# Kernel optimization log

Hardware: AMD Instinct MI355X
Metric: run time of the kernel (lower is better)

## Reference

```python
import jax, jax.numpy as jnp
import numpy as np


def _depthwise3x3(x_nhwc, w):
    # w: (3, 3, 1, C) — depthwise conv, padding=1, matches torch Conv2d(groups=C)
    return jax.lax.conv_general_dilated(
        x_nhwc, w, window_strides=(1, 1), padding='SAME',
        dimension_numbers=('NHWC', 'HWIO', 'NHWC'),
        feature_group_count=x_nhwc.shape[-1])


def _stripe_attn(q, k, v, lepe_w, B, H, W, nh, hd, ss, axis, scale):
    # q/k/v: (B, H, W, nh*hd); axis 0 = horizontal stripes, 1 = vertical
    pad_h = (-H) % ss if axis == 0 else 0
    pad_w = (-W) % ss if axis == 1 else 0
    if pad_h or pad_w:
        pad = ((0, 0), (0, pad_h), (0, pad_w), (0, 0))
        q, k, v = jnp.pad(q, pad), jnp.pad(k, pad), jnp.pad(v, pad)
    Hp, Wp = q.shape[1], q.shape[2]
    lepe = _depthwise3x3(v, lepe_w)  # (B, Hp, Wp, nh*hd)

    if axis == 0:
        nS = Hp // ss
        def to_win(t):  # -> (B*nS*Wp, nh, ss, hd)
            t = t.reshape(B, nS, ss, Wp, nh, hd)
            return t.transpose(0, 1, 3, 4, 2, 5).reshape(B * nS * Wp, nh, ss, hd)
    else:
        nS = Wp // ss
        def to_win(t):  # -> (B*Hp*nS, nh, ss, hd)
            t = t.reshape(B, Hp, nS, ss, nh, hd)
            return t.transpose(0, 1, 2, 4, 3, 5).reshape(B * Hp * nS, nh, ss, hd)

    qw, kw, vw, lw = to_win(q), to_win(k), to_win(v), to_win(lepe)
    attn = jax.nn.softmax(jnp.einsum('wnqd,wnkd->wnqk', qw, kw) / scale, axis=-1)
    out = jnp.einsum('wnqk,wnkd->wnqd', attn, vw) + lw  # (Wnum, nh, ss, hd)

    if axis == 0:
        out = out.transpose(0, 2, 1, 3).reshape(B, nS, Wp, ss, nh * hd)
        out = out.transpose(0, 1, 3, 2, 4).reshape(B, Hp, Wp, nh * hd)
    else:
        out = out.transpose(0, 2, 1, 3).reshape(B, Hp, nS, ss, nh * hd)
        out = out.reshape(B, Hp, Wp, nh * hd)
    return out[:, :H, :W, :].reshape(B, H * W, nh * hd)


def setup_inputs() -> dict:
    key = jax.random.key(0)
    ks = jax.random.split(key, 6)
    B, H, W, dim, n_heads, ss = 8, 64, 64, 512, 16, 8
    half = dim // 2
    x = jax.random.normal(ks[0], (B, H * W, dim), dtype=jnp.float32)
    w_qkv = jax.random.normal(ks[1], (3 * dim, dim), dtype=jnp.float32) * 0.02
    w_proj = jax.random.normal(ks[2], (dim, dim), dtype=jnp.float32) * 0.02
    b_proj = jnp.zeros((dim,), dtype=jnp.float32)
    lepe_h_w = jax.random.normal(ks[3], (3, 3, 1, half), dtype=jnp.float32) * 0.1
    lepe_v_w = jax.random.normal(ks[4], (3, 3, 1, half), dtype=jnp.float32) * 0.1
    return {"x": x, "w_qkv": w_qkv, "w_proj": w_proj, "b_proj": b_proj,
            "lepe_h_w": lepe_h_w, "lepe_v_w": lepe_v_w, "H": H, "W": W}


def reference(x, w_qkv, w_proj, b_proj, lepe_h_w, lepe_v_w, H, W):
    B, L, C = x.shape
    n_heads, ss = 16, 8
    hd = C // n_heads
    scale = float(np.sqrt(hd))
    qkv = x @ w_qkv.T  # (B, L, 3C)
    q, k, v = jnp.split(qkv, 3, axis=-1)
    q = q.reshape(B, H, W, C)
    k = k.reshape(B, H, W, C)
    v = v.reshape(B, H, W, C)
    half = C // 2
    nh_h = n_heads // 2
    nh_v = n_heads - nh_h
    out_h = _stripe_attn(q[..., :half], k[..., :half], v[..., :half],
                         lepe_h_w, B, H, W, nh_h, hd, ss, axis=0, scale=scale)
    out_v = _stripe_attn(q[..., half:], k[..., half:], v[..., half:],
                         lepe_v_w, B, H, W, nh_v, hd, ss, axis=1, scale=scale)
    out = jnp.concatenate([out_h, out_v], axis=-1)
    return out @ w_proj.T + b_proj
```

## Files before the change

kernel.cpp:

```cpp
#include <hip/hip_runtime.h>
#include <hip/hip_bf16.h>
#include <stdint.h>

typedef _Float16 half2v __attribute__((ext_vector_type(2)));
typedef _Float16 half8v __attribute__((ext_vector_type(8)));
typedef uint32_t u32x4  __attribute__((ext_vector_type(4)));
typedef float    f32x4  __attribute__((ext_vector_type(4)));

__device__ __forceinline__ unsigned short f2h(float f) {
  _Float16 h = (_Float16)f;
  return __builtin_bit_cast(unsigned short, h);
}
__device__ __forceinline__ half2v bch2(uint32_t u) {
  return __builtin_bit_cast(half2v, u);
}
__device__ __forceinline__ uint32_t pkrtz_u32(float a, float b) {
  return __builtin_bit_cast(uint32_t, __builtin_amdgcn_cvt_pkrtz(a, b));
}

__device__ __forceinline__ int qkv_idx(int half, int b, int n, int h, int w) {
  int idx = half * 8388608 + (b * 8 + n) * 131072;
  idx += (half == 0) ? ((h >> 3) * 16384 + w * 256 + (h & 7) * 32)
                     : (h * 2048 + w * 32);
  return idx;
}

#define GLOAD_LDS16(gsrc, lbase)                                          \
  __builtin_amdgcn_global_load_lds(                                       \
      (const __attribute__((address_space(1))) uint32_t*)(gsrc),          \
      (__attribute__((address_space(3))) uint32_t*)(lbase), 16, 0, 0)

__global__ __launch_bounds__(256) void cvt_all(
    const float* __restrict__ x,
    const float* __restrict__ wqkv, const float* __restrict__ wproj,
    const float* __restrict__ lh,   const float* __restrict__ lv,
    unsigned short* __restrict__ ox,
    unsigned short* __restrict__ owqkv, unsigned short* __restrict__ owproj,
    unsigned short* __restrict__ owlep)
{
  int i = blockIdx.x * 256 + threadIdx.x;
  const float* src; unsigned short* dst; int off;
  if (i < 4194304)      { src = x;     dst = ox;           off = i; }
  else if ((i -= 4194304) < 196608) { src = wqkv;  dst = owqkv;  off = i; }
  else if ((i -= 196608) < 65536)   { src = wproj; dst = owproj; off = i; }
  else if ((i -= 65536) < 576)      { src = lh;    dst = owlep;  off = i; }
  else if ((i -= 576) < 576)        { src = lv;    dst = owlep + 2304; off = i; }
  else return;
  float4 f = reinterpret_cast<const float4*>(src)[off];
  ushort4 u;
  u.x = f2h(f.x); u.y = f2h(f.y); u.z = f2h(f.z); u.w = f2h(f.w);
  reinterpret_cast<ushort4*>(dst)[off] = u;
}

template<int MODE>
__global__ __launch_bounds__(512, 2) void gemm8(
    const unsigned short* __restrict__ A,
    const unsigned short* __restrict__ Bm,
    unsigned short* __restrict__ Cq,
    float* __restrict__ Cf,
    const float* __restrict__ bias,
    int M, int N)
{
  constexpr int K = 512;
  constexpr int NIT = 4;
  __shared__ unsigned short As[2][256 * 64];
  __shared__ unsigned short Bs[2][256 * 64];
  const int tid  = threadIdx.x;
  const int gn   = N >> 8;
  const int cpx  = gridDim.x >> 3;
  const int bid  = blockIdx.x;
  const int wgid = (bid & 7) * cpx + (bid >> 3);
  const int m0   = (wgid / gn) * 256;
  const int n0   = (wgid % gn) * 256;
  const int wave = tid >> 6, lane = tid & 63;
  const int wr  = wave >> 2;
  const int wcn = wave & 3;

  const int srow = tid >> 3;
  const int schk = ((tid & 7) ^ (srow & 7)) * 8;
  const size_t aSrc = (size_t)(m0 + srow) * K + schk;
  const size_t bSrc = (size_t)(n0 + srow) * K + schk;
  char* ldsA = (char*)(&As[0][0]) + (tid & ~63) * 16;
  char* ldsB = (char*)(&Bs[0][0]) + (tid & ~63) * 16;

#define SA_U(b, kt, u)                                                      \
  GLOAD_LDS16(A + aSrc + (size_t)(u) * 64 * K + (size_t)(kt) * 64,          \
              ldsA + (b) * 32768 + (u) * 8192)
#define SB_U(b, kt, u)                                                      \
  GLOAD_LDS16(Bm + bSrc + (size_t)(u) * 64 * K + (size_t)(kt) * 64,         \
              ldsB + (b) * 32768 + (u) * 8192)
#define BARS                                                                \
  __builtin_amdgcn_s_barrier();                                             \
  __builtin_amdgcn_sched_barrier(0)

  SA_U(0, 0, 0); SA_U(0, 0, 1); SA_U(0, 0, 2); SA_U(0, 0, 3);
  SB_U(0, 0, 0); SB_U(0, 0, 1); SB_U(0, 0, 2); SB_U(0, 0, 3);
  SB_U(1, 1, 0); SB_U(1, 1, 1); SB_U(1, 1, 2); SB_U(1, 1, 3);

  f32x4 acc[8][4];
  const f32x4 zero = {0.f, 0.f, 0.f, 0.f};
  #pragma unroll
  for (int i = 0; i < 8; ++i)
    #pragma unroll
    for (int j = 0; j < 4; ++j) acc[i][j] = zero;

  const int lr  = lane & 15;
  const int kg  = lane >> 4;
  const int ck0 = kg ^ (lr & 7);

  asm volatile("s_waitcnt vmcnt(4)" ::: "memory");
  BARS;

#define LD_AF(buf, mg, ks)                                                  \
  do {                                                                      \
    const unsigned short* ap = &As[buf][0] +                                \
        (wr * 128 + (mg) * 64 + lr) * 64 + (((ks) ? (ck0 ^ 4) : ck0)) * 8;  \
    af[0] = *(const half8v*)(ap);                                           \
    af[1] = *(const half8v*)(ap + 1024);                                    \
    af[2] = *(const half8v*)(ap + 2048);                                    \
    af[3] = *(const half8v*)(ap + 3072);                                    \
  } while (0)
#define LD_BF(buf, ks)                                                      \
  do {                                                                      \
    const unsigned short* bp = &Bs[buf][0] +                                \
        (wcn * 64 + lr) * 64 + (((ks) ? (ck0 ^ 4) : ck0)) * 8;              \
    bf[0] = *(const half8v*)(bp);                                           \
    bf[1] = *(const half8v*)(bp + 1024);                                    \
    bf[2] = *(const half8v*)(bp + 2048);                                    \
    bf[3] = *(const half8v*)(bp + 3072);                                    \
  } while (0)
#define MROW(mg, i)                                                         \
  acc[(mg)*4+(i)][0] = __builtin_amdgcn_mfma_f32_16x16x32_f16(bf[0], af[i], acc[(mg)*4+(i)][0], 0, 0, 0); \
  acc[(mg)*4+(i)][1] = __builtin_amdgcn_mfma_f32_16x16x32_f16(bf[1], af[i], acc[(mg)*4+(i)][1], 0, 0, 0); \
  acc[(mg)*4+(i)][2] = __builtin_amdgcn_mfma_f32_16x16x32_f16(bf[2], af[i], acc[(mg)*4+(i)][2], 0, 0, 0); \
  acc[(mg)*4+(i)][3] = __builtin_amdgcn_mfma_f32_16x16x32_f16(bf[3], af[i], acc[(mg)*4+(i)][3], 0, 0, 0);
#define MFMA16(mg)                                                          \
  do {                                                                      \
    __builtin_amdgcn_s_setprio(1);                                          \
    MROW(mg, 0); MROW(mg, 1); MROW(mg, 2); MROW(mg, 3);                     \
    __builtin_amdgcn_s_setprio(0);                                          \
  } while (0)

  for (int it2 = 0; it2 < NIT; ++it2) {
    const bool more = (it2 + 1 < NIT);
    const int keven = 2 * it2;
    half8v af[4], bf[4];
    LD_BF(0, 0); LD_AF(0, 0, 0);
    SA_U(1, keven + 1, 0); SA_U(1, keven + 1, 1);
    BARS;
    MFMA16(0);
    BARS;
    LD_AF(0, 1, 0);
    SA_U(1, keven + 1, 2); SA_U(1, keven + 1, 3);
    BARS;
    MFMA16(1);
    BARS;
    LD_BF(0, 1); LD_AF(0, 0, 1);
    BARS;
    MFMA16(0);
    BARS;
    LD_AF(0, 1, 1);
    if (more) {
      SB_U(0, keven + 2, 0); SB_U(0, keven + 2, 1);
      asm volatile("s_waitcnt vmcnt(2)" ::: "memory");
    } else {
      asm volatile("s_waitcnt vmcnt(0)" ::: "memory");
    }
    BARS;
    MFMA16(1);
    BARS;
    LD_BF(1, 0); LD_AF(1, 0, 0);
    if (more) { SB_U(0, keven + 2, 2); SB_U(0, keven + 2, 3); }
    BARS;
    MFMA16(0);
    BARS;
    LD_AF(1, 1, 0);
    if (more) { SA_U(0, keven + 2, 0); SA_U(0, keven + 2, 1); }
    BARS;
    MFMA16(1);
    BARS;
    LD_BF(1, 1); LD_AF(1, 0, 1);
    if (more) { SA_U(0, keven + 2, 2); SA_U(0, keven + 2, 3); }
    BARS;
    MFMA16(0);
    BARS;
    LD_AF(1, 1, 1);
    if (more) {
      SB_U(1, keven + 3, 0); SB_U(1, keven + 3, 1);
      SB_U(1, keven + 3, 2); SB_U(1, keven + 3, 3);
      asm volatile("s_waitcnt vmcnt(4)" ::: "memory");
    }
    BARS;
    MFMA16(1);
    BARS;
  }
#undef SA_U
#undef SB_U
#undef LD_AF
#undef LD_BF
#undef MROW
#undef MFMA16
#undef BARS

  const int cr = (lane >> 4) * 4;
  const int cc = lane & 15;

  if constexpr (MODE == 0) {
    #pragma unroll
    for (int j = 0; j < 4; ++j) {
      const int n = n0 + wcn * 64 + j * 16 + cr;
      const float4 b4 = *reinterpret_cast<const float4*>(bias + n);
      #pragma unroll
      for (int i = 0; i < 8; ++i) {
        const int m = m0 + wr * 128 + i * 16 + cc;
        float4 r;
        r.x = acc[i][j][0] + b4.x;
        r.y = acc[i][j][1] + b4.y;
        r.z = acc[i][j][2] + b4.z;
        r.w = acc[i][j][3] + b4.w;
        *reinterpret_cast<float4*>(Cf + (size_t)m * N + n) = r;
      }
    }
  } else {
    const int mb   = m0 + wr * 128;
    const int btok = mb >> 12;
    const int hr0  = (mb >> 6) & 63;
    #pragma unroll
    for (int j = 0; j < 4; ++j) {
      const int nb    = n0 + wcn * 64 + j * 16 + cr;
      const int tq    = nb >> 9;
      const int halfc = (nb >> 8) & 1;
      const int nn    = (nb & 255) >> 5;
      const int ch4   = nb & 31;
      const int headbase = tq * 16777216 + halfc * 8388608 +
                           (btok * 8 + nn) * 131072 + ch4;
      #pragma unroll
      for (int i = 0; i < 8; ++i) {
        const int hrow = hr0 + (i >> 2);
        const int wpix = (i & 3) * 16 + cc;
        const int off = halfc ? (hrow * 2048 + wpix * 32)
                              : ((hrow >> 3) * 16384 + wpix * 256 + (hrow & 7) * 32);
        uint2 r;
        r.x = pkrtz_u32(acc[i][j][0], acc[i][j][1]);
        r.y = pkrtz_u32(acc[i][j][2], acc[i][j][3]);
        *reinterpret_cast<uint2*>(Cq + headbase + off) = r;
      }
    }
  }
}

__global__ __launch_bounds__(256) void gemm_proj(
    const unsigned short* __restrict__ A,
    const unsigned short* __restrict__ B,
    float* __restrict__ Cf,
    const float* __restrict__ bias)
{
  constexpr int K = 512, N = 512;
  __shared__ unsigned short As[2][128 * 32];
  __shared__ unsigned short Bs[2][128 * 32];
  const int tid  = threadIdx.x;
  const int gn   = N >> 7;
  const int cpx  = gridDim.x >> 3;
  const int bid  = blockIdx.x;
  const int wgid = (bid & 7) * cpx + (bid >> 3);
  const int m0   = (wgid / gn) * 128;
  const int n0   = (wgid % gn) * 128;
  const int wave = tid >> 6, lane = tid & 63;
  const int wr = wave >> 1, wc = wave & 1;
  const int sr = tid >> 2;
  const int sc = ((tid & 3) ^ ((tid >> 3) & 3)) * 8;
  const size_t aBase0 = (size_t)(m0 + sr) * K + sc;
  const size_t aBase1 = (size_t)(m0 + 64 + sr) * K + sc;
  const size_t bBase0 = (size_t)(n0 + sr) * K + sc;
  const size_t bBase1 = (size_t)(n0 + 64 + sr) * K + sc;
  char* ldsA = (char*)(&As[0][0]) + (tid & ~63) * 16;
  char* ldsB = (char*)(&Bs[0][0]) + (tid & ~63) * 16;

#define STAGE_P(bsel, kofs)                                        \
  do {                                                             \
    GLOAD_LDS16(A + aBase0 + (kofs), ldsA + (bsel) * 8192);        \
    GLOAD_LDS16(A + aBase1 + (kofs), ldsA + (bsel) * 8192 + 4096); \
    GLOAD_LDS16(B + bBase0 + (kofs), ldsB + (bsel) * 8192);        \
    GLOAD_LDS16(B + bBase1 + (kofs), ldsB + (bsel) * 8192 + 4096); \
  } while (0)

  STAGE_P(0, 0);

  f32x4 acc[4][4];
  const f32x4 zero = {0.f, 0.f, 0.f, 0.f};
  #pragma unroll
  for (int i = 0; i < 4; ++i)
    #pragma unroll
    for (int j = 0; j < 4; ++j) acc[i][j] = zero;

  const int lr   = lane & 15;
  const int slot = (lane >> 4) ^ ((lr >> 1) & 3);

  auto compute = [&](const unsigned short* Asb, const unsigned short* Bsb) {
    half8v af[4], bfr[4];
    #pragma unroll
    for (int i = 0; i < 4; ++i)
      af[i] = *reinterpret_cast<const half8v*>(Asb + (wr * 64 + i * 16 + lr) * 32 + slot * 8);
    #pragma unroll
    for (int j = 0; j < 4; ++j)
      bfr[j] = *reinterpret_cast<const half8v*>(Bsb + (wc * 64 + j * 16 + lr) * 32 + slot * 8);
    __builtin_amdgcn_s_setprio(1);
    #pragma unroll
    for (int i = 0; i < 4; ++i)
      #pragma unroll
      for (int j = 0; j < 4; ++j)
        acc[i][j] = __builtin_amdgcn_mfma_f32_16x16x32_f16(bfr[j], af[i], acc[i][j], 0, 0, 0);
    __builtin_amdgcn_s_setprio(0);
  };

  const int nt = K >> 5;
  for (int t = 0; t < nt - 1; ++t) {
    STAGE_P((t + 1) & 1, (t + 1) * 32);
    asm volatile("s_waitcnt vmcnt(4)" ::: "memory");
    __builtin_amdgcn_s_barrier();
    __builtin_amdgcn_sched_barrier(0);
    compute(&As[t & 1][0], &Bs[t & 1][0]);
    __builtin_amdgcn_s_barrier();
    __builtin_amdgcn_sched_barrier(0);
  }
  asm volatile("s_waitcnt vmcnt(0)" ::: "memory");
  __builtin_amdgcn_s_barrier();
  __builtin_amdgcn_sched_barrier(0);
  compute(&As[(nt - 1) & 1][0], &Bs[(nt - 1) & 1][0]);
#undef STAGE_P

  const int cr = (lane >> 4) * 4;
  const int cc = lane & 15;
  #pragma unroll
  for (int j = 0; j < 4; ++j) {
    const int n = n0 + wc * 64 + j * 16 + cr;
    const float4 b4 = *reinterpret_cast<const float4*>(bias + n);
    #pragma unroll
    for (int i = 0; i < 4; ++i) {
      const int m = m0 + wr * 64 + i * 16 + cc;
      float4 r;
      r.x = acc[i][j][0] + b4.x;
      r.y = acc[i][j][1] + b4.y;
      r.z = acc[i][j][2] + b4.z;
      r.w = acc[i][j][3] + b4.w;
      *reinterpret_cast<float4*>(Cf + (size_t)m * N + n) = r;
    }
  }
}

__global__ __launch_bounds__(256) void attn_lepe(
    const unsigned short* __restrict__ qkvp,
    const unsigned short* __restrict__ wlep,
    unsigned short* __restrict__ outp)
{
  const int gw   = (int)((blockIdx.x * 256 + threadIdx.x) >> 6);
  const int lane = threadIdx.x & 63;
  const int half = gw >> 14;
  const int id   = gw & 16383;
  const int b    = id >> 11;
  const int n    = (id >> 8) & 7;
  int h0, w0;
  if (half == 0) { h0 = ((id >> 5) & 7) * 8; w0 = (id & 31) * 2; }
  else           { h0 = ((id >> 3) & 31) * 2; w0 = (id & 7) * 8; }
  const int baseA = qkv_idx(half, b, n, h0, w0);
  const int dWin  = (half == 0) ? 256 : 2048;
  const int baseB = baseA + dWin;

  const int qr = lane >> 3, kr = lane & 7;
  const unsigned short* qA = qkvp + baseA + qr * 32;
  const unsigned short* kA = qkvp + 16777216 + baseA + kr * 32;
  float sA = 0.f, sB = 0.f;
  #pragma unroll
  for (int c = 0; c < 4; ++c) {
    const u32x4 qa = *reinterpret_cast<const u32x4*>(qA + c * 8);
    const u32x4 ka = *reinterpret_cast<const u32x4*>(kA + c * 8);
    const u32x4 qb = *reinterpret_cast<const u32x4*>(qA + dWin + c * 8);
    const u32x4 kb = *reinterpret_cast<const u32x4*>(kA + dWin + c * 8);
    #pragma unroll
    for (int e = 0; e < 4; ++e) {
      sA = __builtin_amdgcn_fdot2(bch2(qa[e]), bch2(ka[e]), sA, false);
      sB = __builtin_amdgcn_fdot2(bch2(qb[e]), bch2(kb[e]), sB, false);
    }
  }
  const float scl = 0.17677669529663687f;
  const float pA = __expf(sA * scl);
  const float pB = __expf(sB * scl);
  float denA = pA, denB = pB;
  denA += __shfl_xor(denA, 1); denA += __shfl_xor(denA, 2); denA += __shfl_xor(denA, 4);
  denB += __shfl_xor(denB, 1); denB += __shfl_xor(denB, 2); denB += __shfl_xor(denB, 4);
  const float aAv = pA * __builtin_amdgcn_rcpf(denA);
  const float aBv = pB * __builtin_amdgcn_rcpf(denB);
  const uint32_t adu = pkrtz_u32(aAv, aBv);

  const int dgrp = lane & 3;
  const int win  = (lane >> 2) & 1;
  const int qr2  = lane >> 3;
  const int d0   = dgrp * 8;
  const int mybase = win ? baseB : baseA;
  const unsigned short* vwin = qkvp + 33554432 + mybase;

  half2v o01 = {0,0}, o23 = {0,0}, o45 = {0,0}, o67 = {0,0};
  #pragma unroll
  for (int k = 0; k < 8; ++k) {
    const uint32_t pairw = (uint32_t)__shfl((int)adu, qr2 * 8 + k);
    const half2v ph = bch2(pairw);
    const _Float16 av = win ? ph.y : ph.x;
    const half2v ak2 = {av, av};
    const u32x4 vv = *reinterpret_cast<const u32x4*>(vwin + k * 32 + d0);
    o01 += ak2 * bch2(vv[0]);
    o23 += ak2 * bch2(vv[1]);
    o45 += ak2 * bch2(vv[2]);
    o67 += ak2 * bch2(vv[3]);
  }

  const int hq = (half == 0) ? (h0 + qr2) : (h0 + win);
  const int wq = (half == 0) ? (w0 + win) : (w0 + qr2);
  const unsigned short* vplane = qkvp + 33554432;
  const unsigned short* wl = wlep + half * 2304 + n * 32 + d0;
  half2v l01 = {0,0}, l23 = {0,0}, l45 = {0,0}, l67 = {0,0};
  #pragma unroll
  for (int dy = -1; dy <= 1; ++dy) {
    #pragma unroll
    for (int dx = -1; dx <= 1; ++dx) {
      const int hh = hq + dy, ww = wq + dx;
      u32x4 vv = {0u, 0u, 0u, 0u};
      if ((unsigned)hh < 64u && (unsigned)ww < 64u)
        vv = *reinterpret_cast<const u32x4*>(vplane + qkv_idx(half, b, n, hh, ww) + d0);
      const u32x4 wt = *reinterpret_cast<const u32x4*>(wl + ((dy + 1) * 3 + dx + 1) * 256);
      l01 += bch2(wt[0]) * bch2(vv[0]);
      l23 += bch2(wt[1]) * bch2(vv[1]);
      l45 += bch2(wt[2]) * bch2(vv[2]);
      l67 += bch2(wt[3]) * bch2(vv[3]);
    }
  }

  const int m = b * 4096 + hq * 64 + wq;
  const int chan0 = half * 256 + n * 32;
  u32x4 r;
  r[0] = __builtin_bit_cast(uint32_t, (half2v)(o01 + l01));
  r[1] = __builtin_bit_cast(uint32_t, (half2v)(o23 + l23));
  r[2] = __builtin_bit_cast(uint32_t, (half2v)(o45 + l45));
  r[3] = __builtin_bit_cast(uint32_t, (half2v)(o67 + l67));
  *reinterpret_cast<u32x4*>(outp + (size_t)m * 512 + chan0 + d0) = r;
}

extern "C" void kernel_launch(void* const* d_in, const int* in_sizes, int n_in,
                              void* d_out, int out_size, void* d_ws, size_t ws_size,
                              hipStream_t stream) {
  const float* x      = (const float*)d_in[0];
  const float* w_qkv  = (const float*)d_in[1];
  const float* w_proj = (const float*)d_in[2];
  const float* b_proj = (const float*)d_in[3];
  const float* lepe_h = (const float*)d_in[4];
  const float* lepe_v = (const float*)d_in[5];
  float* out = (float*)d_out;

  char* ws = (char*)d_ws;
  unsigned short* qkv_p   = (unsigned short*)ws;
  unsigned short* xh      = (unsigned short*)(ws + 100663296);
  unsigned short* wqkv_h  = (unsigned short*)(ws + 134217728);
  unsigned short* wproj_h = (unsigned short*)(ws + 135790592);
  unsigned short* wlep_h  = (unsigned short*)(ws + 136314880);

  cvt_all<<<17413, 256, 0, stream>>>(x, w_qkv, w_proj, lepe_h, lepe_v,
                                     xh, wqkv_h, wproj_h, wlep_h);

  gemm8<1><<<768, 512, 0, stream>>>(
      xh, wqkv_h, qkv_p, nullptr, nullptr, 32768, 1536);

  attn_lepe<<<8192, 256, 0, stream>>>(qkv_p, wlep_h, xh);

  gemm_proj<<<1024, 256, 0, stream>>>(xh, wproj_h, out, b_proj);
}
```

Measured before the change: 172.5 us.

## Make QKV GEMM persistent over three N tiles with prefetch during epilogue

The QKV GEMM now launches 256 workgroups instead of 768. Each workgroup processes three consecutive 256-wide N tiles for one M tile, so block launch and prologue costs are paid once per workgroup. The next tile's A and B loads are issued before the current tile's epilogue stores, which overlaps the store phase with global-to-LDS prefetch. The cost is lower parallelism: 256 blocks on a 256-CU part gives a single wave of work with no tail balancing, and A is re-read three times per block, though likely from cache.

Result: no change. 169.8 us, median of 2 (-1.6%).

```diff
diff --git a/kernel.cpp b/kernel.cpp
--- a/kernel.cpp
+++ b/kernel.cpp
@@ -52,26 +52,22 @@
   reinterpret_cast<ushort4*>(dst)[off] = u;
 }
 
-template<int MODE>
-__global__ __launch_bounds__(512, 2) void gemm8(
+__global__ __launch_bounds__(512, 2) void gemm8p(
     const unsigned short* __restrict__ A,
     const unsigned short* __restrict__ Bm,
-    unsigned short* __restrict__ Cq,
-    float* __restrict__ Cf,
-    const float* __restrict__ bias,
-    int M, int N)
+    unsigned short* __restrict__ Cq)
 {
   constexpr int K = 512;
   constexpr int NIT = 4;
   __shared__ unsigned short As[2][256 * 64];
   __shared__ unsigned short Bs[2][256 * 64];
   const int tid  = threadIdx.x;
-  const int gn   = N >> 8;
   const int cpx  = gridDim.x >> 3;
   const int bid  = blockIdx.x;
   const int wgid = (bid & 7) * cpx + (bid >> 3);
-  const int m0   = (wgid / gn) * 256;
-  const int n0   = (wgid % gn) * 256;
+  const int mt   = wgid >> 1;
+  const int nh   = wgid & 1;
+  const int m0   = mt * 256;
   const int wave = tid >> 6, lane = tid & 63;
   const int wr  = wave >> 2;
   const int wcn = wave & 3;
@@ -79,37 +75,29 @@
   const int srow = tid >> 3;
   const int schk = ((tid & 7) ^ (srow & 7)) * 8;
   const size_t aSrc = (size_t)(m0 + srow) * K + schk;
-  const size_t bSrc = (size_t)(n0 + srow) * K + schk;
+  size_t bSrc = (size_t)(nh * 768 + srow) * K + schk;
   char* ldsA = (char*)(&As[0][0]) + (tid & ~63) * 16;
   char* ldsB = (char*)(&Bs[0][0]) + (tid & ~63) * 16;
 
 #define SA_U(b, kt, u)                                                      \
   GLOAD_LDS16(A + aSrc + (size_t)(u) * 64 * K + (size_t)(kt) * 64,          \
               ldsA + (b) * 32768 + (u) * 8192)
-#define SB_U(b, kt, u)                                                      \
-  GLOAD_LDS16(Bm + bSrc + (size_t)(u) * 64 * K + (size_t)(kt) * 64,         \
+#define SB_U(b, kt, u, bS)                                                  \
+  GLOAD_LDS16(Bm + (bS) + (size_t)(u) * 64 * K + (size_t)(kt) * 64,         \
               ldsB + (b) * 32768 + (u) * 8192)
 #define BARS                                                                \
   __builtin_amdgcn_s_barrier();                                             \
   __builtin_amdgcn_sched_barrier(0)
 
   SA_U(0, 0, 0); SA_U(0, 0, 1); SA_U(0, 0, 2); SA_U(0, 0, 3);
-  SB_U(0, 0, 0); SB_U(0, 0, 1); SB_U(0, 0, 2); SB_U(0, 0, 3);
-  SB_U(1, 1, 0); SB_U(1, 1, 1); SB_U(1, 1, 2); SB_U(1, 1, 3);
-
-  f32x4 acc[8][4];
-  const f32x4 zero = {0.f, 0.f, 0.f, 0.f};
-  #pragma unroll
-  for (int i = 0; i < 8; ++i)
-    #pragma unroll
-    for (int j = 0; j < 4; ++j) acc[i][j] = zero;
+  SB_U(0, 0, 0, bSrc); SB_U(0, 0, 1, bSrc); SB_U(0, 0, 2, bSrc); SB_U(0, 0, 3, bSrc);
+  SB_U(1, 1, 0, bSrc); SB_U(1, 1, 1, bSrc); SB_U(1, 1, 2, bSrc); SB_U(1, 1, 3, bSrc);
+  asm volatile("s_waitcnt vmcnt(4)" ::: "memory");
+  BARS;
 
   const int lr  = lane & 15;
   const int kg  = lane >> 4;
   const int ck0 = kg ^ (lr & 7);
-
-  asm volatile("s_waitcnt vmcnt(4)" ::: "memory");
-  BARS;
 
 #define LD_AF(buf, mg, ks)                                                  \
   do {                                                                      \
@@ -141,58 +129,112 @@
     __builtin_amdgcn_s_setprio(0);                                          \
   } while (0)
 
-  for (int it2 = 0; it2 < NIT; ++it2) {
-    const bool more = (it2 + 1 < NIT);
-    const int keven = 2 * it2;
-    half8v af[4], bf[4];
-    LD_BF(0, 0); LD_AF(0, 0, 0);
-    SA_U(1, keven + 1, 0); SA_U(1, keven + 1, 1);
-    BARS;
-    MFMA16(0);
-    BARS;
-    LD_AF(0, 1, 0);
-    SA_U(1, keven + 1, 2); SA_U(1, keven + 1, 3);
-    BARS;
-    MFMA16(1);
-    BARS;
-    LD_BF(0, 1); LD_AF(0, 0, 1);
-    BARS;
-    MFMA16(0);
-    BARS;
-    LD_AF(0, 1, 1);
-    if (more) {
-      SB_U(0, keven + 2, 0); SB_U(0, keven + 2, 1);
-      asm volatile("s_waitcnt vmcnt(2)" ::: "memory");
-    } else {
+  f32x4 acc[8][4];
+  const f32x4 zero = {0.f, 0.f, 0.f, 0.f};
+
+  #pragma unroll 1
+  for (int pass = 0; pass < 3; ++pass) {
+    const int n0 = (nh * 3 + pass) * 256;
+    #pragma unroll
+    for (int i = 0; i < 8; ++i)
+      #pragma unroll
+      for (int j = 0; j < 4; ++j) acc[i][j] = zero;
+
+    for (int it2 = 0; it2 < NIT; ++it2) {
+      const bool more = (it2 + 1 < NIT);
+      const int keven = 2 * it2;
+      half8v af[4], bf[4];
+      LD_BF(0, 0); LD_AF(0, 0, 0);
+      SA_U(1, keven + 1, 0); SA_U(1, keven + 1, 1);
+      BARS;
+      MFMA16(0);
+      BARS;
+      LD_AF(0, 1, 0);
+      SA_U(1, keven + 1, 2); SA_U(1, keven + 1, 3);
+      BARS;
+      MFMA16(1);
+      BARS;
+      LD_BF(0, 1); LD_AF(0, 0, 1);
+      BARS;
+      MFMA16(0);
+      BARS;
+      LD_AF(0, 1, 1);
+      if (more) {
+        SB_U(0, keven + 2, 0, bSrc); SB_U(0, keven + 2, 1, bSrc);
+        asm volatile("s_waitcnt vmcnt(2)" ::: "memory");
+      } else {
+        asm volatile("s_waitcnt vmcnt(0)" ::: "memory");
+      }
+      BARS;
+      MFMA16(1);
+      BARS;
+      LD_BF(1, 0); LD_AF(1, 0, 0);
+      if (more) { SB_U(0, keven + 2, 2, bSrc); SB_U(0, keven + 2, 3, bSrc); }
+      BARS;
+      MFMA16(0);
+      BARS;
+      LD_AF(1, 1, 0);
+      if (more) { SA_U(0, keven + 2, 0); SA_U(0, keven + 2, 1); }
+      BARS;
+      MFMA16(1);
+      BARS;
+      LD_BF(1, 1); LD_AF(1, 0, 1);
+      if (more) { SA_U(0, keven + 2, 2); SA_U(0, keven + 2, 3); }
+      BARS;
+      MFMA16(0);
+      BARS;
+      LD_AF(1, 1, 1);
+      if (more) {
+        SB_U(1, keven + 3, 0, bSrc); SB_U(1, keven + 3, 1, bSrc);
+        SB_U(1, keven + 3, 2, bSrc); SB_U(1, keven + 3, 3, bSrc);
+        asm volatile("s_waitcnt vmcnt(4)" ::: "memory");
+      }
+      BARS;
+      MFMA16(1);
+      BARS;
+    }
+
+    if (pass < 2) {
+      const size_t bSrcN = bSrc + (size_t)256 * K;
+      SA_U(0, 0, 0); SA_U(0, 0, 1); SA_U(0, 0, 2); SA_U(0, 0, 3);
+      SB_U(0, 0, 0, bSrcN); SB_U(0, 0, 1, bSrcN); SB_U(0, 0, 2, bSrcN); SB_U(0, 0, 3, bSrcN);
+      SB_U(1, 1, 0, bSrcN); SB_U(1, 1, 1, bSrcN); SB_U(1, 1, 2, bSrcN); SB_U(1, 1, 3, bSrcN);
+      bSrc = bSrcN;
+    }
+
+    {
+      const int cr = (lane >> 4) * 4;
+      const int cc = lane & 15;
+      const int mb   = m0 + wr * 128;
+      const int btok = mb >> 12;
+      const int hr0  = (mb >> 6) & 63;
+      #pragma unroll
+      for (int j = 0; j < 4; ++j) {
+        const int nb    = n0 + wcn * 64 + j * 16 + cr;
+        const int tq    = nb >> 9;
+        const int halfc = (nb >> 8) & 1;
+        const int nn    = (nb & 255) >> 5;
+        const int ch4   = nb & 31;
+        const int headbase = tq * 16777216 + halfc * 8388608 +
+                             (btok * 8 + nn) * 131072 + ch4;
+        #pragma unroll
+        for (int i = 0; i < 8; ++i) {
+          const int hrow = hr0 + (i >> 2);
+          const int wpix = (i & 3) * 16 + cc;
+          const int off = halfc ? (hrow * 2048 + wpix * 32)
+                                : ((hrow >> 3) * 16384 + wpix * 256 + (hrow & 7) * 32);
+          uint2 r;
+          r.x = pkrtz_u32(acc[i][j][0], acc[i][j][1]);
+          r.y = pkrtz_u32(acc[i][j][2], acc[i][j][3]);
+          *reinterpret_cast<uint2*>(Cq + headbase + off) = r;
+        }
+      }
+    }
+
+    if (pass < 2) {
       asm volatile("s_waitcnt vmcnt(0)" ::: "memory");
-    }
-    BARS;
-    MFMA16(1);
-    BARS;
-    LD_BF(1, 0); LD_AF(1, 0, 0);
-    if (more) { SB_U(0, keven + 2, 2); SB_U(0, keven + 2, 3); }
-    BARS;
-    MFMA16(0);
-    BARS;
-    LD_AF(1, 1, 0);
-    if (more) { SA_U(0, keven + 2, 0); SA_U(0, keven + 2, 1); }
-    BARS;
-    MFMA16(1);
-    BARS;
-    LD_BF(1, 1); LD_AF(1, 0, 1);
-    if (more) { SA_U(0, keven + 2, 2); SA_U(0, keven + 2, 3); }
-    BARS;
-    MFMA16(0);
-    BARS;
-    LD_AF(1, 1, 1);
-    if (more) {
-      SB_U(1, keven + 3, 0); SB_U(1, keven + 3, 1);
-      SB_U(1, keven + 3, 2); SB_U(1, keven + 3, 3);
-      asm volatile("s_waitcnt vmcnt(4)" ::: "memory");
-    }
-    BARS;
-    MFMA16(1);
-    BARS;
+      BARS;
+    }
   }
 #undef SA_U
 #undef SB_U
@@ -201,52 +243,6 @@
 #undef MROW
 #undef MFMA16
 #undef BARS
-
-  const int cr = (lane >> 4) * 4;
-  const int cc = lane & 15;
-
-  if constexpr (MODE == 0) {
-    #pragma unroll
-    for (int j = 0; j < 4; ++j) {
-      const int n = n0 + wcn * 64 + j * 16 + cr;
-      const float4 b4 = *reinterpret_cast<const float4*>(bias + n);
-      #pragma unroll
-      for (int i = 0; i < 8; ++i) {
-        const int m = m0 + wr * 128 + i * 16 + cc;
-        float4 r;
-        r.x = acc[i][j][0] + b4.x;
-        r.y = acc[i][j][1] + b4.y;
-        r.z = acc[i][j][2] + b4.z;
-        r.w = acc[i][j][3] + b4.w;
-        *reinterpret_cast<float4*>(Cf + (size_t)m * N + n) = r;
-      }
-    }
-  } else {
-    const int mb   = m0 + wr * 128;
-    const int btok = mb >> 12;
-    const int hr0  = (mb >> 6) & 63;
-    #pragma unroll
-    for (int j = 0; j < 4; ++j) {
-      const int nb    = n0 + wcn * 64 + j * 16 + cr;
-      const int tq    = nb >> 9;
-      const int halfc = (nb >> 8) & 1;
-      const int nn    = (nb & 255) >> 5;
-      const int ch4   = nb & 31;
-      const int headbase = tq * 16777216 + halfc * 8388608 +
-                           (btok * 8 + nn) * 131072 + ch4;
-      #pragma unroll
-      for (int i = 0; i < 8; ++i) {
-        const int hrow = hr0 + (i >> 2);
-        const int wpix = (i & 3) * 16 + cc;
-        const int off = halfc ? (hrow * 2048 + wpix * 32)
-                              : ((hrow >> 3) * 16384 + wpix * 256 + (hrow & 7) * 32);
-        uint2 r;
-        r.x = pkrtz_u32(acc[i][j][0], acc[i][j][1]);
-        r.y = pkrtz_u32(acc[i][j][2], acc[i][j][3]);
-        *reinterpret_cast<uint2*>(Cq + headbase + off) = r;
-      }
-    }
-  }
 }
 
 __global__ __launch_bounds__(256) void gemm_proj(
@@ -465,8 +461,7 @@
   cvt_all<<<17413, 256, 0, stream>>>(x, w_qkv, w_proj, lepe_h, lepe_v,
                                      xh, wqkv_h, wproj_h, wlep_h);
 
-  gemm8<1><<<768, 512, 0, stream>>>(
-      xh, wqkv_h, qkv_p, nullptr, nullptr, 32768, 1536);
+  gemm8p<<<256, 512, 0, stream>>>(xh, wqkv_h, qkv_p);
 
   attn_lepe<<<8192, 256, 0, stream>>>(qkv_p, wlep_h, xh);
 
```
